# Performance work log

Hardware: AMD Instinct MI355X
Metric: run time of the kernel (lower is better)

## Reference

```python
import jax, jax.numpy as jnp
import numpy as np

H = 1024          # hidden_size
A = 8             # num_actions
T = 64            # timesteps
N = 256           # batch (num envs)


def _gru_cell(x, h, Wih, Whh, bih, bhh):
    # torch.nn.GRUCell math; gate order (r, z, n)
    gi = x @ Wih.T + bih           # [N, 3H]
    gh = h @ Whh.T + bhh           # [N, 3H]
    i_r, i_z, i_n = jnp.split(gi, 3, axis=1)
    h_r, h_z, h_n = jnp.split(gh, 3, axis=1)
    r = jax.nn.sigmoid(i_r + h_r)
    z = jax.nn.sigmoid(i_z + h_z)
    n = jnp.tanh(i_n + r * h_n)
    return (1.0 - z) * n + z * h


def setup_inputs() -> dict:
    key = jax.random.key(0)
    ks = jax.random.split(key, 12)
    s = 0.02
    return {
        "c": jax.random.normal(ks[0], (T * N, H), jnp.float32),
        "hxs": jax.random.normal(ks[1], (N, 3 * H), jnp.float32),
        "masks": jnp.ones((T * N, 1), jnp.float32),
        "prev_action_one_hot": jnp.zeros((T * N, A), jnp.float32).at[jnp.arange(T * N), jax.random.randint(ks[2], (T * N,), 0, A)].set(1.0),
        "h_gru_Wih": s * jax.random.normal(ks[3], (3 * H, H), jnp.float32),
        "h_gru_Whh": s * jax.random.normal(ks[4], (3 * H, H), jnp.float32),
        "h_gru_bih": jnp.zeros((3 * H,), jnp.float32),
        "h_gru_bhh": jnp.zeros((3 * H,), jnp.float32),
        "f_gru_Wih": s * jax.random.normal(ks[5], (3 * H, H), jnp.float32),
        "f_gru_Whh": s * jax.random.normal(ks[6], (3 * H, H), jnp.float32),
        "f_gru_bih": jnp.zeros((3 * H,), jnp.float32),
        "f_gru_bhh": jnp.zeros((3 * H,), jnp.float32),
        "p_W": s * jax.random.normal(ks[7], (2 * H, 2 * H + A), jnp.float32),
        "p_b": jnp.zeros((2 * H,), jnp.float32),
        "q_W": s * jax.random.normal(ks[8], (2 * H, 2 * H + A), jnp.float32),
        "q_b": jnp.zeros((2 * H,), jnp.float32),
    }


def reference(c, hxs, masks, prev_action_one_hot,
              h_gru_Wih, h_gru_Whh, h_gru_bih, h_gru_bhh,
              f_gru_Wih, f_gru_Whh, f_gru_bih, f_gru_bhh,
              p_W, p_b, q_W, q_b):
    c3 = c.reshape(T, N, H)
    m3 = masks.reshape(T, N, 1)
    a3 = prev_action_one_hot.reshape(T, N, A)
    f0 = hxs[:, :H]
    h0 = hxs[:, H:2 * H]
    q0 = hxs[:, 2 * H:]

    def step(carry, xs):
        f, h, q_mu = carry
        c_t, m_t, a_t = xs
        p_in = jnp.concatenate([h, q_mu, a_t], axis=1) * m_t
        p_dist = p_in @ p_W.T + p_b                     # [N, 2H]
        p_mu = p_dist[:, :H]
        q_in = jnp.concatenate([f, c_t, a_t], axis=1) * m_t
        q_dist = q_in @ q_W.T + q_b                     # [N, 2H]
        q_mu_new = q_dist[:, :H]
        f_new = _gru_cell(c_t, f * m_t, f_gru_Wih, f_gru_Whh, f_gru_bih, f_gru_bhh)
        h_new = _gru_cell(p_mu, h * m_t, h_gru_Wih, h_gru_Whh, h_gru_bih, h_gru_bhh)
        return (f_new, h_new, q_mu_new), (p_dist, q_dist)

    (f, h, q_mu), (p_all, q_all) = jax.lax.scan(step, (f0, h0, q0), (c3, m3, a3))
    acc_p = p_all.reshape(T * N, 2 * H)
    acc_q = q_all.reshape(T * N, 2 * H)
    hxs_out = jnp.concatenate([f, h, q_mu], axis=1)
    return acc_p, acc_q, hxs_out
```

## Files before the change

kernel.cpp:

```cpp
#include <hip/hip_runtime.h>
#include <math.h>

typedef __attribute__((ext_vector_type(8))) __bf16 bf16x8;
typedef __attribute__((ext_vector_type(4))) float f32x4;

constexpr int H = 1024, T = 64, NB = 256, TWOH = 2048, THREEH = 3072;
constexpr long long OFF_Q  = 33554432LL;
constexpr long long OFF_HX = 67108864LL;
constexpr int LA = 6;

constexpr int R_PWH = 0, R_PWQ = 2048, R_QWF = 4096, R_QWC = 6144,
              R_FWIH = 8192, R_FWHH = 11264, R_HWIH = 14336, R_HWHH = 17408;

#define LD4(p) (*reinterpret_cast<const float4*>(p))

__device__ __forceinline__ float sigf(float x) { return 1.0f / (1.0f + expf(-x)); }

__device__ __forceinline__ void gload16(const void* g, void* l) {
    __builtin_amdgcn_global_load_lds(
        (const __attribute__((address_space(1))) uint32_t*)g,
        (__attribute__((address_space(3))) uint32_t*)l, 16, 0, 0);
}

__device__ __forceinline__ void st_bf_swz(__bf16* base, int n, int k, float v) {
    base[(size_t)n * 1024 + (((k >> 3) ^ (n & 7)) << 3) + (k & 7)] = (__bf16)v;
}

#define FRAGOFF(rloc, gl) (((rloc) << 7) + ((((gl)) ^ ((rloc) & 7)) << 4))

template<int RT>
__device__ __forceinline__ void stage_tile(const char* g, char* l, int kb, int tid) {
    #pragma unroll
    for (int i = 0; i < RT / 32; ++i) {
        const int L = i * 4096 + tid * 16;
        gload16(g + (size_t)(L >> 7) * 2048 + (size_t)kb * 128 + (L & 127), l + L);
    }
}

__device__ __forceinline__ void mm128(
    int tid, char* sA, char* sB,
    const char* A0, const char* B0, int n0,
    const char* A1, const char* B1, int n1,
    f32x4 (&acc)[2][4])
{
    const int lane = tid & 63, w = tid >> 6;
    const int l15 = lane & 15, lg = lane >> 4;
    const int wr = w >> 1, wc = w & 1;
    const int nit = n0 + n1;
    int aoff[2][2], boff[4][2];
    #pragma unroll
    for (int fr = 0; fr < 2; ++fr)
        #pragma unroll
        for (int kk = 0; kk < 2; ++kk)
            aoff[fr][kk] = FRAGOFF(wr * 32 + fr * 16 + l15, kk * 4 + lg);
    #pragma unroll
    for (int fc = 0; fc < 4; ++fc)
        #pragma unroll
        for (int kk = 0; kk < 2; ++kk)
            boff[fc][kk] = FRAGOFF(wc * 64 + fc * 16 + l15, kk * 4 + lg);

    stage_tile<64>(A0, sA, 0, tid);
    stage_tile<128>(B0, sB, 0, tid);
    for (int kb = 0; kb < nit; ++kb) {
        const int kn = kb + 1;
        if (kn < nit) {
            const char* An = (kn < n0) ? A0 : A1;
            const char* Bn = (kn < n0) ? B0 : B1;
            const int kl = (kn < n0) ? kn : kn - n0;
            stage_tile<64>(An, sA + (kn & 1) * 8192, kl, tid);
            stage_tile<128>(Bn, sB + (kn & 1) * 16384, kl, tid);
            asm volatile("s_waitcnt vmcnt(6)" ::: "memory");
        } else {
            asm volatile("s_waitcnt vmcnt(0)" ::: "memory");
        }
        __builtin_amdgcn_s_barrier();
        __builtin_amdgcn_sched_barrier(0);
        char* Ab = sA + (kb & 1) * 8192;
        char* Bb = sB + (kb & 1) * 16384;
        bf16x8 af[2][2], bv[4][2];
        #pragma unroll
        for (int fr = 0; fr < 2; ++fr)
            #pragma unroll
            for (int kk = 0; kk < 2; ++kk)
                af[fr][kk] = *reinterpret_cast<const bf16x8*>(Ab + aoff[fr][kk]);
        #pragma unroll
        for (int fc = 0; fc < 4; ++fc)
            #pragma unroll
            for (int kk = 0; kk < 2; ++kk)
                bv[fc][kk] = *reinterpret_cast<const bf16x8*>(Bb + boff[fc][kk]);
        __builtin_amdgcn_s_setprio(1);
        #pragma unroll
        for (int kk = 0; kk < 2; ++kk)
            #pragma unroll
            for (int fr = 0; fr < 2; ++fr)
                #pragma unroll
                for (int fc = 0; fc < 4; ++fc)
                    acc[fr][fc] = __builtin_amdgcn_mfma_f32_16x16x32_bf16(
                        af[fr][kk], bv[fc][kk], acc[fr][fc], 0, 0, 0);
        __builtin_amdgcn_s_setprio(0);
        __builtin_amdgcn_s_barrier();
        __builtin_amdgcn_sched_barrier(0);
    }
}

__device__ __forceinline__ void mm32g1(
    int tid, char* sA, char* sB,
    const char* A, const char* Bg,
    f32x4 (&aR)[2], f32x4 (&aZ)[2], f32x4 (&aN)[2])
{
    const int lane = tid & 63, w = tid >> 6;
    const int l15 = lane & 15, lg = lane >> 4;
    const int wr = w >> 1, wc = w & 1;
    int aoff[2], boff[2][2];
    #pragma unroll
    for (int kk = 0; kk < 2; ++kk)
        aoff[kk] = FRAGOFF(wr * 16 + l15, kk * 4 + lg);
    #pragma unroll
    for (int fc = 0; fc < 2; ++fc)
        #pragma unroll
        for (int kk = 0; kk < 2; ++kk)
            boff[fc][kk] = FRAGOFF(wc * 32 + fc * 16 + l15, kk * 4 + lg);

    auto stg = [&](int buf, int kb) {
        stage_tile<32>(A, sA + buf * 4096, kb, tid);
        #pragma unroll
        for (int g = 0; g < 3; ++g)
            stage_tile<64>(Bg + (size_t)g * 2097152, sB + buf * 24576 + g * 8192, kb, tid);
    };
    stg(0, 0);
    for (int kb = 0; kb < 16; ++kb) {
        if (kb + 1 < 16) {
            stg((kb + 1) & 1, kb + 1);
            asm volatile("s_waitcnt vmcnt(7)" ::: "memory");
        } else {
            asm volatile("s_waitcnt vmcnt(0)" ::: "memory");
        }
        __builtin_amdgcn_s_barrier();
        __builtin_amdgcn_sched_barrier(0);
        char* Ab = sA + (kb & 1) * 4096;
        char* Bb = sB + (kb & 1) * 24576;
        bf16x8 af[2];
        #pragma unroll
        for (int kk = 0; kk < 2; ++kk)
            af[kk] = *reinterpret_cast<const bf16x8*>(Ab + aoff[kk]);
        bf16x8 bvr[2][2], bvz[2][2], bvn[2][2];
        #pragma unroll
        for (int fc = 0; fc < 2; ++fc)
            #pragma unroll
            for (int kk = 0; kk < 2; ++kk) {
                bvr[fc][kk] = *reinterpret_cast<const bf16x8*>(Bb + boff[fc][kk]);
                bvz[fc][kk] = *reinterpret_cast<const bf16x8*>(Bb + 8192 + boff[fc][kk]);
                bvn[fc][kk] = *reinterpret_cast<const bf16x8*>(Bb + 16384 + boff[fc][kk]);
            }
        __builtin_amdgcn_s_setprio(1);
        #pragma unroll
        for (int kk = 0; kk < 2; ++kk)
            #pragma unroll
            for (int fc = 0; fc < 2; ++fc) {
                aR[fc] = __builtin_amdgcn_mfma_f32_16x16x32_bf16(af[kk], bvr[fc][kk], aR[fc], 0, 0, 0);
                aZ[fc] = __builtin_amdgcn_mfma_f32_16x16x32_bf16(af[kk], bvz[fc][kk], aZ[fc], 0, 0, 0);
                aN[fc] = __builtin_amdgcn_mfma_f32_16x16x32_bf16(af[kk], bvn[fc][kk], aN[fc], 0, 0, 0);
            }
        __builtin_amdgcn_s_setprio(0);
        __builtin_amdgcn_s_barrier();
        __builtin_amdgcn_sched_barrier(0);
    }
}

__device__ __forceinline__ void do_xq(int slice, int i, int tid, char* sA, char* sB,
    const char* cbfB, const char* Wb, const float* act, const float* qW, float* out)
{
    const int lane = tid & 63, w = tid >> 6;
    const int l15 = lane & 15, lg = lane >> 4;
    const int wr = w >> 1, wc = w & 1;
    const int row0 = (i >> 4) * 64, col0 = (i & 15) * 128;
    const size_t grow0 = (size_t)slice * NB + row0;
    f32x4 acc[2][4] = {};
    mm128(tid, sA, sB, cbfB + grow0 * 2048, Wb + (size_t)(R_QWC + col0) * 2048, 16,
          nullptr, nullptr, 0, acc);
    #pragma unroll
    for (int fc = 0; fc < 4; ++fc) {
        const int gc = col0 + wc * 64 + fc * 16 + l15;
        const float* wp = qW + (size_t)gc * 2056 + 2048;
        float4 x0 = LD4(wp), x1 = LD4(wp + 4);
        #pragma unroll
        for (int fr = 0; fr < 2; ++fr)
            #pragma unroll
            for (int j = 0; j < 4; ++j) {
                const size_t n = grow0 + wr * 32 + fr * 16 + lg * 4 + j;
                const float* ar = act + n * 8;
                float4 a0 = LD4(ar), a1 = LD4(ar + 4);
                float dot = a0.x * x0.x + a0.y * x0.y + a0.z * x0.z + a0.w * x0.w
                          + a1.x * x1.x + a1.y * x1.y + a1.z * x1.z + a1.w * x1.w;
                out[OFF_Q + n * TWOH + gc] = acc[fr][fc][j] + dot;
            }
    }
}

__device__ __forceinline__ void do_gf(int slice, int i, int tid, char* sA, char* sB,
    const char* cbfB, const char* Wb, __bf16* Gfb)
{
    const int lane = tid & 63, w = tid >> 6;
    const int l15 = lane & 15, lg = lane >> 4;
    const int wr = w >> 1, wc = w & 1;
    const int row0 = (i / 24) * 64, col0 = (i % 24) * 128;
    f32x4 acc[2][4] = {};
    mm128(tid, sA, sB, cbfB + ((size_t)slice * NB + row0) * 2048,
          Wb + (size_t)(R_FWIH + col0) * 2048, 16, nullptr, nullptr, 0, acc);
    __bf16* gdst = Gfb + (size_t)(slice & 7) * NB * THREEH;
    #pragma unroll
    for (int fc = 0; fc < 4; ++fc) {
        const int gc = col0 + wc * 64 + fc * 16 + l15;
        #pragma unroll
        for (int fr = 0; fr < 2; ++fr)
            #pragma unroll
            for (int j = 0; j < 4; ++j) {
                const int n = row0 + wr * 32 + fr * 16 + lg * 4 + j;
                gdst[(size_t)n * THREEH + gc] = (__bf16)acc[fr][fc][j];
            }
    }
}

__global__ __launch_bounds__(256) void wcvt_k(
    const float* __restrict__ pW, const float* __restrict__ qW,
    const float* __restrict__ fWih, const float* __restrict__ fWhh,
    const float* __restrict__ hWih, const float* __restrict__ hWhh,
    __bf16* __restrict__ Wbf)
{
    const long i = (long)blockIdx.x * 256 + threadIdx.x;
    const int row = (int)(i >> 7);
    const int G   = (int)i & 127;
    const float* src; int stride; int koff = 0; int r;
    if (row < 2048)       { src = pW;   stride = 2056; koff = 0;    r = row; }
    else if (row < 4096)  { src = pW;   stride = 2056; koff = 1024; r = row - 2048; }
    else if (row < 6144)  { src = qW;   stride = 2056; koff = 0;    r = row - 4096; }
    else if (row < 8192)  { src = qW;   stride = 2056; koff = 1024; r = row - 6144; }
    else if (row < 11264) { src = fWih; stride = 1024; r = row - 8192; }
    else if (row < 14336) { src = fWhh; stride = 1024; r = row - 11264; }
    else if (row < 17408) { src = hWih; stride = 1024; r = row - 14336; }
    else                  { src = hWhh; stride = 1024; r = row - 17408; }
    const float* p = src + (long)r * stride + koff + G * 8;
    float4 a = LD4(p), b = LD4(p + 4);
    bf16x8 v;
    v[0] = (__bf16)a.x; v[1] = (__bf16)a.y; v[2] = (__bf16)a.z; v[3] = (__bf16)a.w;
    v[4] = (__bf16)b.x; v[5] = (__bf16)b.y; v[6] = (__bf16)b.z; v[7] = (__bf16)b.w;
    *reinterpret_cast<bf16x8*>(Wbf + (size_t)row * 1024 + ((G ^ (row & 7)) << 3)) = v;
}

__global__ __launch_bounds__(256) void ccvt_k(const float* __restrict__ c,
                                              __bf16* __restrict__ cbf) {
    const long i = (long)blockIdx.x * 256 + threadIdx.x;
    const int row = (int)(i >> 7);
    const int G   = (int)i & 127;
    const float* p = c + (size_t)row * 1024 + G * 8;
    float4 a = LD4(p), b = LD4(p + 4);
    bf16x8 v;
    v[0] = (__bf16)a.x; v[1] = (__bf16)a.y; v[2] = (__bf16)a.z; v[3] = (__bf16)a.w;
    v[4] = (__bf16)b.x; v[5] = (__bf16)b.y; v[6] = (__bf16)b.z; v[7] = (__bf16)b.w;
    *reinterpret_cast<bf16x8*>(cbf + (size_t)row * 1024 + ((G ^ (row & 7)) << 3)) = v;
}

__global__ __launch_bounds__(256) void init2_k(
    const float* __restrict__ hxs, const float* __restrict__ masks,
    float* __restrict__ fst0, float* __restrict__ hst0,
    __bf16* __restrict__ fbm0, __bf16* __restrict__ hbm0, __bf16* __restrict__ qmub0)
{
    const int idx = blockIdx.x * 256 + threadIdx.x;
    const int arr = idx >> 15;
    const int g   = idx & 32767;
    const int n   = g >> 7;
    const int G   = g & 127;
    const float m0 = masks[n];
    const float* p = hxs + (size_t)n * THREEH + arr * 1024 + G * 8;
    float4 a = LD4(p), b = LD4(p + 4);
    __bf16* dstB = arr == 0 ? fbm0 : (arr == 1 ? hbm0 : qmub0);
    bf16x8 v;
    v[0] = (__bf16)(a.x * m0); v[1] = (__bf16)(a.y * m0);
    v[2] = (__bf16)(a.z * m0); v[3] = (__bf16)(a.w * m0);
    v[4] = (__bf16)(b.x * m0); v[5] = (__bf16)(b.y * m0);
    v[6] = (__bf16)(b.z * m0); v[7] = (__bf16)(b.w * m0);
    *reinterpret_cast<bf16x8*>(dstB + (size_t)n * 1024 + ((G ^ (n & 7)) << 3)) = v;
    if (arr < 2) {
        float* dstF = arr == 0 ? fst0 : hst0;
        *reinterpret_cast<float4*>(dstF + (size_t)n * 1024 + G * 8) = a;
        *reinterpret_cast<float4*>(dstF + (size_t)n * 1024 + G * 8 + 4) = b;
    }
}

__global__ __launch_bounds__(256) void pre_k(
    const char* __restrict__ cbfB, const char* __restrict__ Wb,
    const float* __restrict__ act, const float* __restrict__ qW,
    __bf16* __restrict__ Gfb, float* __restrict__ out)
{
    __shared__ char smem[49152];
    const int s = blockIdx.x / 160;
    const int i = blockIdx.x % 160;
    if (i < 64) do_xq(s, i, threadIdx.x, smem, smem + 16384, cbfB, Wb, act, qW, out);
    else        do_gf(s, i - 64, threadIdx.x, smem, smem + 16384, cbfB, Wb, Gfb);
}

__global__ __launch_bounds__(256) void k1_k(
    int t, int hasFiller,
    const __bf16* __restrict__ hbm, const __bf16* __restrict__ qmub,
    __bf16* __restrict__ qmubN,
    const __bf16* __restrict__ fbm, const char* __restrict__ cbfB,
    const float* __restrict__ masks, const float* __restrict__ act,
    const float* __restrict__ pW, const float* __restrict__ pb,
    const float* __restrict__ qb, const float* __restrict__ qW,
    const char* __restrict__ Wb,
    __bf16* __restrict__ pmub, float* __restrict__ Shh, __bf16* __restrict__ Gfb,
    float* __restrict__ out)
{
    __shared__ char smem[49152];
    char* sA = smem;
    char* sB = smem + 16384;
    const int tid = threadIdx.x;
    const int lane = tid & 63, w = tid >> 6;
    const int l15 = lane & 15, lg = lane >> 4;
    const int wr = w >> 1, wc = w & 1;
    const float* mrow = masks + (size_t)t * NB;
    const float* mn   = masks + (size_t)(t + 1 < T ? t + 1 : t) * NB;
    int b = blockIdx.x;

    if (b < 64) {
        const int row0 = (b >> 4) * 64, col0 = (b & 15) * 128;
        f32x4 acc[2][4] = {};
        mm128(tid, sA, sB,
              (const char*)hbm + (size_t)row0 * 2048, Wb + (size_t)(R_PWH + col0) * 2048, 16,
              (const char*)qmub + (size_t)row0 * 2048, Wb + (size_t)(R_PWQ + col0) * 2048, 16,
              acc);
        float* ob = out + (size_t)t * NB * TWOH;
        #pragma unroll
        for (int fc = 0; fc < 4; ++fc) {
            const int gc = col0 + wc * 64 + fc * 16 + l15;
            const float* wp = pW + (size_t)gc * 2056 + 2048;
            float4 x0 = LD4(wp), x1 = LD4(wp + 4);
            const float bb = pb[gc];
            #pragma unroll
            for (int fr = 0; fr < 2; ++fr)
                #pragma unroll
                for (int j = 0; j < 4; ++j) {
                    const int n = row0 + wr * 32 + fr * 16 + lg * 4 + j;
                    const float* ar = act + ((size_t)t * NB + n) * 8;
                    float4 a0 = LD4(ar), a1 = LD4(ar + 4);
                    float dot = a0.x * x0.x + a0.y * x0.y + a0.z * x0.z + a0.w * x0.w
                              + a1.x * x1.x + a1.y * x1.y + a1.z * x1.z + a1.w * x1.w;
                    float v = acc[fr][fc][j] + mrow[n] * dot + bb;
                    ob[(size_t)n * TWOH + gc] = v;
                    if (gc < 1024) st_bf_swz(pmub, n, gc, v);
                }
        }
    } else if (b < 128) {
        b -= 64;
        const int row0 = (b >> 4) * 64, col0 = (b & 15) * 128;
        f32x4 acc[2][4] = {};
        mm128(tid, sA, sB,
              (const char*)fbm + (size_t)row0 * 2048, Wb + (size_t)(R_QWF + col0) * 2048, 16,
              nullptr, nullptr, 0, acc);
        float* ob = out + OFF_Q + (size_t)t * NB * TWOH;
        #pragma unroll
        for (int fc = 0; fc < 4; ++fc) {
            const int gc = col0 + wc * 64 + fc * 16 + l15;
            const float bb = qb[gc];
            #pragma unroll
            for (int fr = 0; fr < 2; ++fr)
                #pragma unroll
                for (int j = 0; j < 4; ++j) {
                    const int n = row0 + wr * 32 + fr * 16 + lg * 4 + j;
                    const float xq = ob[(size_t)n * TWOH + gc];
                    float v = acc[fr][fc][j] + mrow[n] * xq + bb;
                    ob[(size_t)n * TWOH + gc] = v;
                    if (gc < 1024) st_bf_swz(qmubN, n, gc, v * mn[n]);
                }
        }
    } else if (b < 224) {
        const int i = b - 128;
        const int row0 = (i / 24) * 64, col0 = (i % 24) * 128;
        f32x4 acc[2][4] = {};
        mm128(tid, sA, sB,
              (const char*)hbm + (size_t)row0 * 2048, Wb + (size_t)(R_HWHH + col0) * 2048, 16,
              nullptr, nullptr, 0, acc);
        #pragma unroll
        for (int fc = 0; fc < 4; ++fc) {
            const int gc = col0 + wc * 64 + fc * 16 + l15;
            #pragma unroll
            for (int fr = 0; fr < 2; ++fr)
                #pragma unroll
                for (int j = 0; j < 4; ++j) {
                    const int n = row0 + wr * 32 + fr * 16 + lg * 4 + j;
                    Shh[(size_t)n * THREEH + gc] = acc[fr][fc][j];
                }
        }
    } else if (b < 288) {
        if (hasFiller) do_xq(t + LA, b - 224, tid, sA, sB, cbfB, Wb, act, qW, out);
    } else {
        if (hasFiller) do_gf(t + LA, b - 288, tid, sA, sB, cbfB, Wb, Gfb);
    }
}

__global__ __launch_bounds__(256) void k2_k(
    int t,
    const __bf16* __restrict__ pmub, const __bf16* __restrict__ hbm,
    const __bf16* __restrict__ fbm,
    const float* __restrict__ Shh, const __bf16* __restrict__ Gfb,
    const float* __restrict__ hstF, float* __restrict__ hstN, __bf16* __restrict__ hbmN,
    const float* __restrict__ fstF, float* __restrict__ fstN, __bf16* __restrict__ fbmN,
    const char* __restrict__ Wb,
    const float* __restrict__ hbih, const float* __restrict__ hbhh,
    const float* __restrict__ fbih, const float* __restrict__ fbhh,
    const float* __restrict__ masks)
{
    __shared__ char smem[57344];
    char* sA = smem;
    char* sB = smem + 8192;
    const int tid = threadIdx.x;
    const int lane = tid & 63, w = tid >> 6;
    const int l15 = lane & 15, lg = lane >> 4;
    const int wr = w >> 1, wc = w & 1;
    const float* mrow = masks + (size_t)t * NB;
    const float* mn   = masks + (size_t)(t + 1 < T ? t + 1 : t) * NB;
    const int b = blockIdx.x;
    const int i = b & 127;
    const int row0 = (i >> 4) * 32, col0 = (i & 15) * 64;

    f32x4 aR[2] = {}, aZ[2] = {}, aN[2] = {};
    if (b < 128) {
        mm32g1(tid, sA, sB,
               (const char*)pmub + (size_t)row0 * 2048,
               Wb + (size_t)(R_HWIH + col0) * 2048, aR, aZ, aN);
        #pragma unroll
        for (int fc = 0; fc < 2; ++fc) {
            const int col = col0 + wc * 32 + fc * 16 + l15;
            const float bri = hbih[col],        brh = hbhh[col];
            const float bzi = hbih[col + 1024], bzh = hbhh[col + 1024];
            const float bni = hbih[col + 2048], bnh = hbhh[col + 2048];
            #pragma unroll
            for (int j = 0; j < 4; ++j) {
                const int n = row0 + wr * 16 + lg * 4 + j;
                const float ghr = Shh[(size_t)n * THREEH + col];
                const float ghz = Shh[(size_t)n * THREEH + col + 1024];
                const float ghn = Shh[(size_t)n * THREEH + col + 2048];
                const float rg = sigf(aR[fc][j] + bri + ghr + brh);
                const float zg = sigf(aZ[fc][j] + bzi + ghz + bzh);
                const float ng = tanhf(aN[fc][j] + bni + rg * (ghn + bnh));
                const float hm = hstF[(size_t)n * 1024 + col] * mrow[n];
                const float o = (1.f - zg) * ng + zg * hm;
                hstN[(size_t)n * 1024 + col] = o;
                st_bf_swz(hbmN, n, col, o * mn[n]);
            }
        }
    } else {
        mm32g1(tid, sA, sB,
               (const char*)fbm + (size_t)row0 * 2048,
               Wb + (size_t)(R_FWHH + col0) * 2048, aR, aZ, aN);
        const __bf16* gsl = Gfb + (size_t)(t & 7) * NB * THREEH;
        #pragma unroll
        for (int fc = 0; fc < 2; ++fc) {
            const int col = col0 + wc * 32 + fc * 16 + l15;
            const float br  = fbih[col] + fbhh[col];
            const float bz  = fbih[col + 1024] + fbhh[col + 1024];
            const float bni = fbih[col + 2048], bnh = fbhh[col + 2048];
            #pragma unroll
            for (int j = 0; j < 4; ++j) {
                const int n = row0 + wr * 16 + lg * 4 + j;
                const float gfr = (float)gsl[(size_t)n * THREEH + col];
                const float gfz = (float)gsl[(size_t)n * THREEH + col + 1024];
                const float gfn = (float)gsl[(size_t)n * THREEH + col + 2048];
                const float rg = sigf(gfr + aR[fc][j] + br);
                const float zg = sigf(gfz + aZ[fc][j] + bz);
                const float ng = tanhf(gfn + bni + rg * (aN[fc][j] + bnh));
                const float fm = fstF[(size_t)n * 1024 + col] * mrow[n];
                const float o = (1.f - zg) * ng + zg * fm;
                fstN[(size_t)n * 1024 + col] = o;
                st_bf_swz(fbmN, n, col, o * mn[n]);
            }
        }
    }
}

__global__ __launch_bounds__(256) void write_hxs_k(const float* __restrict__ fS,
                                                   const float* __restrict__ hS,
                                                   float* out) {
    const int i = blockIdx.x * 256 + threadIdx.x;
    const int n = i / THREEH;
    const int j = i - n * THREEH;
    float v;
    if (j < H)          v = fS[(size_t)n * H + j];
    else if (j < TWOH)  v = hS[(size_t)n * H + (j - H)];
    else                v = out[OFF_Q + ((size_t)(T - 1) * NB + n) * TWOH + (j - TWOH)];
    out[OFF_HX + i] = v;
}

extern "C" void kernel_launch(void* const* d_in, const int* in_sizes, int n_in,
                              void* d_out, int out_size, void* d_ws, size_t ws_size,
                              hipStream_t stream) {
    (void)in_sizes; (void)n_in; (void)out_size; (void)ws_size;

    const float* c     = (const float*)d_in[0];
    const float* hxs   = (const float*)d_in[1];
    const float* masks = (const float*)d_in[2];
    const float* act   = (const float*)d_in[3];
    const float* hWih  = (const float*)d_in[4];
    const float* hWhh  = (const float*)d_in[5];
    const float* hbih  = (const float*)d_in[6];
    const float* hbhh  = (const float*)d_in[7];
    const float* fWih  = (const float*)d_in[8];
    const float* fWhh  = (const float*)d_in[9];
    const float* fbih  = (const float*)d_in[10];
    const float* fbhh  = (const float*)d_in[11];
    const float* pW    = (const float*)d_in[12];
    const float* pb    = (const float*)d_in[13];
    const float* qW    = (const float*)d_in[14];
    const float* qb    = (const float*)d_in[15];

    float* out = (float*)d_out;
    char*  wsb = (char*)d_ws;

    __bf16* Wbf  = (__bf16*)(wsb);
    __bf16* cbf  = (__bf16*)(wsb + 41943040LL);
    float*  fst[2] = { (float*)(wsb + 75497472LL), (float*)(wsb + 76546048LL) };
    float*  hst[2] = { (float*)(wsb + 77594624LL), (float*)(wsb + 78643200LL) };
    __bf16* fbm[2] = { (__bf16*)(wsb + 79691776LL), (__bf16*)(wsb + 80216064LL) };
    __bf16* hbm[2] = { (__bf16*)(wsb + 80740352LL), (__bf16*)(wsb + 81264640LL) };
    __bf16* qmb[2] = { (__bf16*)(wsb + 81788928LL), (__bf16*)(wsb + 82313216LL) };
    __bf16* pmub   = (__bf16*)(wsb + 82837504LL);
    float*  Shh    = (float*)(wsb + 83361792LL);
    __bf16* Gfb    = (__bf16*)(wsb + 86507520LL);
    const char* Wb = (const char*)Wbf;
    const char* cbfB = (const char*)cbf;

    wcvt_k <<<dim3(10240), dim3(256), 0, stream>>>(pW, qW, fWih, fWhh, hWih, hWhh, Wbf);
    ccvt_k <<<dim3(8192),  dim3(256), 0, stream>>>(c, cbf);
    init2_k<<<dim3(384),   dim3(256), 0, stream>>>(hxs, masks, fst[0], hst[0],
                                                   fbm[0], hbm[0], qmb[0]);
    pre_k  <<<dim3(LA * 160), dim3(256), 0, stream>>>(cbfB, Wb, act, qW, Gfb, out);

    for (int t = 0; t < T; ++t) {
        const int cur = t & 1, nxt = cur ^ 1;
        const int hasF = (t + LA < T) ? 1 : 0;
        k1_k<<<dim3(hasF ? 384 : 224), dim3(256), 0, stream>>>(
            t, hasF, hbm[cur], qmb[cur], qmb[nxt], fbm[cur], cbfB,
            masks, act, pW, pb, qb, qW, Wb, pmub, Shh, Gfb, out);
        k2_k<<<dim3(256), dim3(256), 0, stream>>>(
            t, pmub, hbm[cur], fbm[cur], Shh, Gfb,
            hst[cur], hst[nxt], hbm[nxt],
            fst[cur], fst[nxt], fbm[nxt],
            Wb, hbih, hbhh, fbih, fbhh, masks);
    }

    write_hxs_k<<<dim3(3072), dim3(256), 0, stream>>>(fst[0], hst[0], out);
}
```

Before: 2.271 ms.

## Fold p_W into h-GRU input weights and merge per-step kernels into one

Precomputes the products of the h-GRU input weights with the p_W blocks (for h, q_mu, the action columns and the bias) so the h-GRU input gates come straight from h and q_mu with K=3072. This removes the dependency on p_mu within a timestep, so the two per-step launches (k1, k2) collapse into a single step kernel. The Shh and pmub round trips through global memory also go away. The cost is extra precompute kernels, a larger per-step GEMM for the h-GRU blocks, and an additional bf16 rounding of the composed weights that may shift numerics.

```diff
diff --git a/kernel.cpp b/kernel.cpp
--- a/kernel.cpp
+++ b/kernel.cpp
@@ -103,18 +103,24 @@
     }
 }
 
-__device__ __forceinline__ void mm32g1(
+__device__ __forceinline__ void mm64g(
     int tid, char* sA, char* sB,
-    const char* A, const char* Bg,
-    f32x4 (&aR)[2], f32x4 (&aZ)[2], f32x4 (&aN)[2])
+    const char* A0, const char* B0,
+    const char* A1, const char* B1,
+    const char* A2, const char* B2,
+    int nseg, int nhMask,
+    f32x4 (&aR)[2][2], f32x4 (&aZ)[2][2], f32x4 (&aNi)[2][2], f32x4 (&aNh)[2][2])
 {
     const int lane = tid & 63, w = tid >> 6;
     const int l15 = lane & 15, lg = lane >> 4;
     const int wr = w >> 1, wc = w & 1;
-    int aoff[2], boff[2][2];
-    #pragma unroll
-    for (int kk = 0; kk < 2; ++kk)
-        aoff[kk] = FRAGOFF(wr * 16 + l15, kk * 4 + lg);
+    const int nit = nseg * 16;
+    int aoff[2][2], boff[2][2];
+    #pragma unroll
+    for (int fr = 0; fr < 2; ++fr)
+        #pragma unroll
+        for (int kk = 0; kk < 2; ++kk)
+            aoff[fr][kk] = FRAGOFF(wr * 32 + fr * 16 + l15, kk * 4 + lg);
     #pragma unroll
     for (int fc = 0; fc < 2; ++fc)
         #pragma unroll
@@ -122,27 +128,32 @@
             boff[fc][kk] = FRAGOFF(wc * 32 + fc * 16 + l15, kk * 4 + lg);
 
     auto stg = [&](int buf, int kb) {
-        stage_tile<32>(A, sA + buf * 4096, kb, tid);
+        const int seg = kb >> 4, kl = kb & 15;
+        const char* Ag = (seg == 0) ? A0 : ((seg == 1) ? A1 : A2);
+        const char* Bg = (seg == 0) ? B0 : ((seg == 1) ? B1 : B2);
+        stage_tile<64>(Ag, sA + buf * 8192, kl, tid);
         #pragma unroll
         for (int g = 0; g < 3; ++g)
-            stage_tile<64>(Bg + (size_t)g * 2097152, sB + buf * 24576 + g * 8192, kb, tid);
+            stage_tile<64>(Bg + (size_t)g * 2097152, sB + buf * 24576 + g * 8192, kl, tid);
     };
     stg(0, 0);
-    for (int kb = 0; kb < 16; ++kb) {
-        if (kb + 1 < 16) {
+    for (int kb = 0; kb < nit; ++kb) {
+        if (kb + 1 < nit) {
             stg((kb + 1) & 1, kb + 1);
-            asm volatile("s_waitcnt vmcnt(7)" ::: "memory");
+            asm volatile("s_waitcnt vmcnt(8)" ::: "memory");
         } else {
             asm volatile("s_waitcnt vmcnt(0)" ::: "memory");
         }
         __builtin_amdgcn_s_barrier();
         __builtin_amdgcn_sched_barrier(0);
-        char* Ab = sA + (kb & 1) * 4096;
+        char* Ab = sA + (kb & 1) * 8192;
         char* Bb = sB + (kb & 1) * 24576;
-        bf16x8 af[2];
-        #pragma unroll
-        for (int kk = 0; kk < 2; ++kk)
-            af[kk] = *reinterpret_cast<const bf16x8*>(Ab + aoff[kk]);
+        bf16x8 af[2][2];
+        #pragma unroll
+        for (int fr = 0; fr < 2; ++fr)
+            #pragma unroll
+            for (int kk = 0; kk < 2; ++kk)
+                af[fr][kk] = *reinterpret_cast<const bf16x8*>(Ab + aoff[fr][kk]);
         bf16x8 bvr[2][2], bvz[2][2], bvn[2][2];
         #pragma unroll
         for (int fc = 0; fc < 2; ++fc)
@@ -152,15 +163,38 @@
                 bvz[fc][kk] = *reinterpret_cast<const bf16x8*>(Bb + 8192 + boff[fc][kk]);
                 bvn[fc][kk] = *reinterpret_cast<const bf16x8*>(Bb + 16384 + boff[fc][kk]);
             }
+        const bool toNh = (nhMask >> (kb >> 4)) & 1;
         __builtin_amdgcn_s_setprio(1);
         #pragma unroll
         for (int kk = 0; kk < 2; ++kk)
             #pragma unroll
-            for (int fc = 0; fc < 2; ++fc) {
-                aR[fc] = __builtin_amdgcn_mfma_f32_16x16x32_bf16(af[kk], bvr[fc][kk], aR[fc], 0, 0, 0);
-                aZ[fc] = __builtin_amdgcn_mfma_f32_16x16x32_bf16(af[kk], bvz[fc][kk], aZ[fc], 0, 0, 0);
-                aN[fc] = __builtin_amdgcn_mfma_f32_16x16x32_bf16(af[kk], bvn[fc][kk], aN[fc], 0, 0, 0);
-            }
+            for (int fr = 0; fr < 2; ++fr)
+                #pragma unroll
+                for (int fc = 0; fc < 2; ++fc) {
+                    aR[fr][fc] = __builtin_amdgcn_mfma_f32_16x16x32_bf16(
+                        af[fr][kk], bvr[fc][kk], aR[fr][fc], 0, 0, 0);
+                    aZ[fr][fc] = __builtin_amdgcn_mfma_f32_16x16x32_bf16(
+                        af[fr][kk], bvz[fc][kk], aZ[fr][fc], 0, 0, 0);
+                }
+        if (toNh) {
+            #pragma unroll
+            for (int kk = 0; kk < 2; ++kk)
+                #pragma unroll
+                for (int fr = 0; fr < 2; ++fr)
+                    #pragma unroll
+                    for (int fc = 0; fc < 2; ++fc)
+                        aNh[fr][fc] = __builtin_amdgcn_mfma_f32_16x16x32_bf16(
+                            af[fr][kk], bvn[fc][kk], aNh[fr][fc], 0, 0, 0);
+        } else {
+            #pragma unroll
+            for (int kk = 0; kk < 2; ++kk)
+                #pragma unroll
+                for (int fr = 0; fr < 2; ++fr)
+                    #pragma unroll
+                    for (int fc = 0; fc < 2; ++fc)
+                        aNi[fr][fc] = __builtin_amdgcn_mfma_f32_16x16x32_bf16(
+                            af[fr][kk], bvn[fc][kk], aNi[fr][fc], 0, 0, 0);
+        }
         __builtin_amdgcn_s_setprio(0);
         __builtin_amdgcn_s_barrier();
         __builtin_amdgcn_sched_barrier(0);
@@ -258,6 +292,91 @@
     v[0] = (__bf16)a.x; v[1] = (__bf16)a.y; v[2] = (__bf16)a.z; v[3] = (__bf16)a.w;
     v[4] = (__bf16)b.x; v[5] = (__bf16)b.y; v[6] = (__bf16)b.z; v[7] = (__bf16)b.w;
     *reinterpret_cast<bf16x8*>(cbf + (size_t)row * 1024 + ((G ^ (row & 7)) << 3)) = v;
+}
+
+__global__ __launch_bounds__(256) void pwt_k(const float* __restrict__ pW,
+                                             __bf16* __restrict__ pWT) {
+    __shared__ float lds[64][65];
+    const int t = threadIdx.x;
+    const int i0 = blockIdx.y * 64, j0 = blockIdx.x * 64;
+    const int ir = t >> 4, jc = (t & 15) * 4;
+    #pragma unroll
+    for (int rr = 0; rr < 4; ++rr) {
+        const int il = rr * 16 + ir;
+        float4 v = LD4(pW + (size_t)(i0 + il) * 2056 + j0 + jc);
+        lds[jc + 0][il] = v.x; lds[jc + 1][il] = v.y;
+        lds[jc + 2][il] = v.z; lds[jc + 3][il] = v.w;
+    }
+    __syncthreads();
+    #pragma unroll
+    for (int ww = 0; ww < 2; ++ww) {
+        const int jl = ww * 32 + (t >> 3);
+        const int g8 = t & 7;
+        bf16x8 v;
+        #pragma unroll
+        for (int u = 0; u < 8; ++u) v[u] = (__bf16)lds[jl][g8 * 8 + u];
+        const int j = j0 + jl;
+        const int G = (i0 >> 3) + g8;
+        *reinterpret_cast<bf16x8*>(pWT + (size_t)j * 1024 + ((G ^ (j & 7)) << 3)) = v;
+    }
+}
+
+__global__ __launch_bounds__(256) void comp_k(const char* __restrict__ Wb,
+                                              const char* __restrict__ pWTb,
+                                              __bf16* __restrict__ Ch,
+                                              __bf16* __restrict__ Cq) {
+    __shared__ char smem[49152];
+    const int tid = threadIdx.x;
+    const int lane = tid & 63, w = tid >> 6;
+    const int l15 = lane & 15, lg = lane >> 4;
+    const int wr = w >> 1, wc = w & 1;
+    const int row0 = (blockIdx.x >> 4) * 64;
+    const int col0 = (blockIdx.x & 15) * 128;
+    f32x4 acc[2][4] = {};
+    mm128(tid, smem, smem + 16384,
+          Wb + (size_t)(R_HWIH + row0) * 2048, pWTb + (size_t)col0 * 2048, 16,
+          nullptr, nullptr, 0, acc);
+    #pragma unroll
+    for (int fc = 0; fc < 4; ++fc) {
+        const int j = col0 + wc * 64 + fc * 16 + l15;
+        #pragma unroll
+        for (int fr = 0; fr < 2; ++fr)
+            #pragma unroll
+            for (int jj = 0; jj < 4; ++jj) {
+                const int g = row0 + wr * 32 + fr * 16 + lg * 4 + jj;
+                const float v = acc[fr][fc][jj];
+                if (j < 1024) st_bf_swz(Ch, g, j, v);
+                else          st_bf_swz(Cq, g, j - 1024, v);
+            }
+    }
+}
+
+__global__ __launch_bounds__(256) void ca_k(const float* __restrict__ hWih,
+                                            const float* __restrict__ pW,
+                                            const float* __restrict__ pb,
+                                            float* __restrict__ Ca,
+                                            float* __restrict__ cbv) {
+    const int g = blockIdx.x * 4 + (threadIdx.x >> 6);
+    const int l = threadIdx.x & 63;
+    float s[9] = {};
+    for (int it = 0; it < 16; ++it) {
+        const int i = l + it * 64;
+        const float hw = hWih[(size_t)g * 1024 + i];
+        const float* pr = pW + (size_t)i * 2056 + 2048;
+        float4 x0 = LD4(pr), x1 = LD4(pr + 4);
+        s[0] += hw * x0.x; s[1] += hw * x0.y; s[2] += hw * x0.z; s[3] += hw * x0.w;
+        s[4] += hw * x1.x; s[5] += hw * x1.y; s[6] += hw * x1.z; s[7] += hw * x1.w;
+        s[8] += hw * pb[i];
+    }
+    #pragma unroll
+    for (int off = 32; off >= 1; off >>= 1)
+        #pragma unroll
+        for (int u = 0; u < 9; ++u) s[u] += __shfl_down(s[u], off);
+    if (l == 0) {
+        #pragma unroll
+        for (int u = 0; u < 8; ++u) Ca[(size_t)g * 8 + u] = s[u];
+        cbv[g] = s[8];
+    }
 }
 
 __global__ __launch_bounds__(256) void init2_k(
@@ -299,7 +418,7 @@
     else        do_gf(s, i - 64, threadIdx.x, smem, smem + 16384, cbfB, Wb, Gfb);
 }
 
-__global__ __launch_bounds__(256) void k1_k(
+__global__ __launch_bounds__(256) void step_k(
     int t, int hasFiller,
     const __bf16* __restrict__ hbm, const __bf16* __restrict__ qmub,
     __bf16* __restrict__ qmubN,
@@ -307,11 +426,16 @@
     const float* __restrict__ masks, const float* __restrict__ act,
     const float* __restrict__ pW, const float* __restrict__ pb,
     const float* __restrict__ qb, const float* __restrict__ qW,
-    const char* __restrict__ Wb,
-    __bf16* __restrict__ pmub, float* __restrict__ Shh, __bf16* __restrict__ Gfb,
-    float* __restrict__ out)
-{
-    __shared__ char smem[49152];
+    const char* __restrict__ Wb, const char* __restrict__ ChB,
+    const char* __restrict__ CqB,
+    const float* __restrict__ Ca, const float* __restrict__ cbv,
+    const float* __restrict__ hstF, float* __restrict__ hstN, __bf16* __restrict__ hbmN,
+    const float* __restrict__ fstF, float* __restrict__ fstN, __bf16* __restrict__ fbmN,
+    const float* __restrict__ hbih, const float* __restrict__ hbhh,
+    const float* __restrict__ fbih, const float* __restrict__ fbhh,
+    __bf16* __restrict__ Gfb, float* __restrict__ out)
+{
+    __shared__ char smem[65536];
     char* sA = smem;
     char* sB = smem + 16384;
     const int tid = threadIdx.x;
@@ -345,9 +469,7 @@
                     float4 a0 = LD4(ar), a1 = LD4(ar + 4);
                     float dot = a0.x * x0.x + a0.y * x0.y + a0.z * x0.z + a0.w * x0.w
                               + a1.x * x1.x + a1.y * x1.y + a1.z * x1.z + a1.w * x1.w;
-                    float v = acc[fr][fc][j] + mrow[n] * dot + bb;
-                    ob[(size_t)n * TWOH + gc] = v;
-                    if (gc < 1024) st_bf_swz(pmub, n, gc, v);
+                    ob[(size_t)n * TWOH + gc] = acc[fr][fc][j] + mrow[n] * dot + bb;
                 }
         }
     } else if (b < 128) {
@@ -373,86 +495,60 @@
                     if (gc < 1024) st_bf_swz(qmubN, n, gc, v * mn[n]);
                 }
         }
-    } else if (b < 224) {
+    } else if (b < 192) {
         const int i = b - 128;
-        const int row0 = (i / 24) * 64, col0 = (i % 24) * 128;
-        f32x4 acc[2][4] = {};
-        mm128(tid, sA, sB,
-              (const char*)hbm + (size_t)row0 * 2048, Wb + (size_t)(R_HWHH + col0) * 2048, 16,
-              nullptr, nullptr, 0, acc);
-        #pragma unroll
-        for (int fc = 0; fc < 4; ++fc) {
-            const int gc = col0 + wc * 64 + fc * 16 + l15;
+        const int row0 = (i >> 4) * 64, col0 = (i & 15) * 64;
+        f32x4 aR[2][2] = {}, aZ[2][2] = {}, aNi[2][2] = {}, aNh[2][2] = {};
+        mm64g(tid, sA, sB,
+              (const char*)hbm + (size_t)row0 * 2048, ChB + (size_t)col0 * 2048,
+              (const char*)hbm + (size_t)row0 * 2048, Wb + (size_t)(R_HWHH + col0) * 2048,
+              (const char*)qmub + (size_t)row0 * 2048, CqB + (size_t)col0 * 2048,
+              3, 0b010, aR, aZ, aNi, aNh);
+        #pragma unroll
+        for (int fc = 0; fc < 2; ++fc) {
+            const int col = col0 + wc * 32 + fc * 16 + l15;
+            const float cbr = cbv[col]        + hbih[col]        + hbhh[col];
+            const float cbz = cbv[col + 1024] + hbih[col + 1024] + hbhh[col + 1024];
+            const float cbn = cbv[col + 2048] + hbih[col + 2048];
+            const float bnh = hbhh[col + 2048];
+            const float* car = Ca + (size_t)col * 8;
+            const float* caz = Ca + (size_t)(col + 1024) * 8;
+            const float* can = Ca + (size_t)(col + 2048) * 8;
+            float4 r0 = LD4(car), r1 = LD4(car + 4);
+            float4 z0 = LD4(caz), z1 = LD4(caz + 4);
+            float4 n0 = LD4(can), n1 = LD4(can + 4);
             #pragma unroll
             for (int fr = 0; fr < 2; ++fr)
                 #pragma unroll
                 for (int j = 0; j < 4; ++j) {
                     const int n = row0 + wr * 32 + fr * 16 + lg * 4 + j;
-                    Shh[(size_t)n * THREEH + gc] = acc[fr][fc][j];
+                    const float m = mrow[n];
+                    const float* ar = act + ((size_t)t * NB + n) * 8;
+                    float4 a0 = LD4(ar), a1 = LD4(ar + 4);
+                    const float dr = a0.x*r0.x + a0.y*r0.y + a0.z*r0.z + a0.w*r0.w
+                                   + a1.x*r1.x + a1.y*r1.y + a1.z*r1.z + a1.w*r1.w;
+                    const float dz = a0.x*z0.x + a0.y*z0.y + a0.z*z0.z + a0.w*z0.w
+                                   + a1.x*z1.x + a1.y*z1.y + a1.z*z1.z + a1.w*z1.w;
+                    const float dn = a0.x*n0.x + a0.y*n0.y + a0.z*n0.z + a0.w*n0.w
+                                   + a1.x*n1.x + a1.y*n1.y + a1.z*n1.z + a1.w*n1.w;
+                    const float rg = sigf(aR[fr][fc][j] + m * dr + cbr);
+                    const float zg = sigf(aZ[fr][fc][j] + m * dz + cbz);
+                    const float ng = tanhf(aNi[fr][fc][j] + m * dn + cbn
+                                           + rg * (aNh[fr][fc][j] + bnh));
+                    const float hm = hstF[(size_t)n * 1024 + col] * m;
+                    const float o = (1.f - zg) * ng + zg * hm;
+                    hstN[(size_t)n * 1024 + col] = o;
+                    st_bf_swz(hbmN, n, col, o * mn[n]);
                 }
         }
-    } else if (b < 288) {
-        if (hasFiller) do_xq(t + LA, b - 224, tid, sA, sB, cbfB, Wb, act, qW, out);
-    } else {
-        if (hasFiller) do_gf(t + LA, b - 288, tid, sA, sB, cbfB, Wb, Gfb);
-    }
-}
-
-__global__ __launch_bounds__(256) void k2_k(
-    int t,
-    const __bf16* __restrict__ pmub, const __bf16* __restrict__ hbm,
-    const __bf16* __restrict__ fbm,
-    const float* __restrict__ Shh, const __bf16* __restrict__ Gfb,
-    const float* __restrict__ hstF, float* __restrict__ hstN, __bf16* __restrict__ hbmN,
-    const float* __restrict__ fstF, float* __restrict__ fstN, __bf16* __restrict__ fbmN,
-    const char* __restrict__ Wb,
-    const float* __restrict__ hbih, const float* __restrict__ hbhh,
-    const float* __restrict__ fbih, const float* __restrict__ fbhh,
-    const float* __restrict__ masks)
-{
-    __shared__ char smem[57344];
-    char* sA = smem;
-    char* sB = smem + 8192;
-    const int tid = threadIdx.x;
-    const int lane = tid & 63, w = tid >> 6;
-    const int l15 = lane & 15, lg = lane >> 4;
-    const int wr = w >> 1, wc = w & 1;
-    const float* mrow = masks + (size_t)t * NB;
-    const float* mn   = masks + (size_t)(t + 1 < T ? t + 1 : t) * NB;
-    const int b = blockIdx.x;
-    const int i = b & 127;
-    const int row0 = (i >> 4) * 32, col0 = (i & 15) * 64;
-
-    f32x4 aR[2] = {}, aZ[2] = {}, aN[2] = {};
-    if (b < 128) {
-        mm32g1(tid, sA, sB,
-               (const char*)pmub + (size_t)row0 * 2048,
-               Wb + (size_t)(R_HWIH + col0) * 2048, aR, aZ, aN);
-        #pragma unroll
-        for (int fc = 0; fc < 2; ++fc) {
-            const int col = col0 + wc * 32 + fc * 16 + l15;
-            const float bri = hbih[col],        brh = hbhh[col];
-            const float bzi = hbih[col + 1024], bzh = hbhh[col + 1024];
-            const float bni = hbih[col + 2048], bnh = hbhh[col + 2048];
-            #pragma unroll
-            for (int j = 0; j < 4; ++j) {
-                const int n = row0 + wr * 16 + lg * 4 + j;
-                const float ghr = Shh[(size_t)n * THREEH + col];
-                const float ghz = Shh[(size_t)n * THREEH + col + 1024];
-                const float ghn = Shh[(size_t)n * THREEH + col + 2048];
-                const float rg = sigf(aR[fc][j] + bri + ghr + brh);
-                const float zg = sigf(aZ[fc][j] + bzi + ghz + bzh);
-                const float ng = tanhf(aN[fc][j] + bni + rg * (ghn + bnh));
-                const float hm = hstF[(size_t)n * 1024 + col] * mrow[n];
-                const float o = (1.f - zg) * ng + zg * hm;
-                hstN[(size_t)n * 1024 + col] = o;
-                st_bf_swz(hbmN, n, col, o * mn[n]);
-            }
-        }
-    } else {
-        mm32g1(tid, sA, sB,
-               (const char*)fbm + (size_t)row0 * 2048,
-               Wb + (size_t)(R_FWHH + col0) * 2048, aR, aZ, aN);
+    } else if (b < 256) {
+        const int i = b - 192;
+        const int row0 = (i >> 4) * 64, col0 = (i & 15) * 64;
+        f32x4 aR[2][2] = {}, aZ[2][2] = {}, aNi[2][2] = {}, aNh[2][2] = {};
+        mm64g(tid, sA, sB,
+              (const char*)fbm + (size_t)row0 * 2048, Wb + (size_t)(R_FWHH + col0) * 2048,
+              nullptr, nullptr, nullptr, nullptr,
+              1, 0b001, aR, aZ, aNi, aNh);
         const __bf16* gsl = Gfb + (size_t)(t & 7) * NB * THREEH;
         #pragma unroll
         for (int fc = 0; fc < 2; ++fc) {
@@ -461,20 +557,26 @@
             const float bz  = fbih[col + 1024] + fbhh[col + 1024];
             const float bni = fbih[col + 2048], bnh = fbhh[col + 2048];
             #pragma unroll
-            for (int j = 0; j < 4; ++j) {
-                const int n = row0 + wr * 16 + lg * 4 + j;
-                const float gfr = (float)gsl[(size_t)n * THREEH + col];
-                const float gfz = (float)gsl[(size_t)n * THREEH + col + 1024];
-                const float gfn = (float)gsl[(size_t)n * THREEH + col + 2048];
-                const float rg = sigf(gfr + aR[fc][j] + br);
-                const float zg = sigf(gfz + aZ[fc][j] + bz);
-                const float ng = tanhf(gfn + bni + rg * (aN[fc][j] + bnh));
-                const float fm = fstF[(size_t)n * 1024 + col] * mrow[n];
-                const float o = (1.f - zg) * ng + zg * fm;
-                fstN[(size_t)n * 1024 + col] = o;
-                st_bf_swz(fbmN, n, col, o * mn[n]);
-            }
+            for (int fr = 0; fr < 2; ++fr)
+                #pragma unroll
+                for (int j = 0; j < 4; ++j) {
+                    const int n = row0 + wr * 32 + fr * 16 + lg * 4 + j;
+                    const float gfr = (float)gsl[(size_t)n * THREEH + col];
+                    const float gfz = (float)gsl[(size_t)n * THREEH + col + 1024];
+                    const float gfn = (float)gsl[(size_t)n * THREEH + col + 2048];
+                    const float rg = sigf(gfr + aR[fr][fc][j] + br);
+                    const float zg = sigf(gfz + aZ[fr][fc][j] + bz);
+                    const float ng = tanhf(gfn + bni + rg * (aNh[fr][fc][j] + bnh));
+                    const float fm = fstF[(size_t)n * 1024 + col] * mrow[n];
+                    const float o = (1.f - zg) * ng + zg * fm;
+                    fstN[(size_t)n * 1024 + col] = o;
+                    st_bf_swz(fbmN, n, col, o * mn[n]);
+                }
         }
+    } else if (b < 320) {
+        if (hasFiller) do_xq(t + LA, b - 256, tid, sA, sB, cbfB, Wb, act, qW, out);
+    } else {
+        if (hasFiller) do_gf(t + LA, b - 320, tid, sA, sB, cbfB, Wb, Gfb);
     }
 }
 
@@ -523,29 +625,34 @@
     __bf16* fbm[2] = { (__bf16*)(wsb + 79691776LL), (__bf16*)(wsb + 80216064LL) };
     __bf16* hbm[2] = { (__bf16*)(wsb + 80740352LL), (__bf16*)(wsb + 81264640LL) };
     __bf16* qmb[2] = { (__bf16*)(wsb + 81788928LL), (__bf16*)(wsb + 82313216LL) };
-    __bf16* pmub   = (__bf16*)(wsb + 82837504LL);
-    float*  Shh    = (float*)(wsb + 83361792LL);
-    __bf16* Gfb    = (__bf16*)(wsb + 86507520LL);
-    const char* Wb = (const char*)Wbf;
+    __bf16* pWT    = (__bf16*)(wsb + 82837504LL);
+    __bf16* Chbuf  = (__bf16*)(wsb + 87031808LL);
+    __bf16* Cqbuf  = (__bf16*)(wsb + 93323264LL);
+    float*  Ca     = (float*)(wsb + 99614720LL);
+    float*  cbv    = (float*)(wsb + 99713024LL);
+    __bf16* Gfb    = (__bf16*)(wsb + 99725312LL);
+    const char* Wb   = (const char*)Wbf;
     const char* cbfB = (const char*)cbf;
 
     wcvt_k <<<dim3(10240), dim3(256), 0, stream>>>(pW, qW, fWih, fWhh, hWih, hWhh, Wbf);
     ccvt_k <<<dim3(8192),  dim3(256), 0, stream>>>(c, cbf);
+    pwt_k  <<<dim3(32, 16), dim3(256), 0, stream>>>(pW, pWT);
     init2_k<<<dim3(384),   dim3(256), 0, stream>>>(hxs, masks, fst[0], hst[0],
                                                    fbm[0], hbm[0], qmb[0]);
+    comp_k <<<dim3(768), dim3(256), 0, stream>>>(Wb, (const char*)pWT, Chbuf, Cqbuf);
+    ca_k   <<<dim3(768), dim3(256), 0, stream>>>(hWih, pW, pb, Ca, cbv);
     pre_k  <<<dim3(LA * 160), dim3(256), 0, stream>>>(cbfB, Wb, act, qW, Gfb, out);
 
     for (int t = 0; t < T; ++t) {
         const int cur = t & 1, nxt = cur ^ 1;
         const int hasF = (t + LA < T) ? 1 : 0;
-        k1_k<<<dim3(hasF ? 384 : 224), dim3(256), 0, stream>>>(
+        step_k<<<dim3(hasF ? 416 : 256), dim3(256), 0, stream>>>(
             t, hasF, hbm[cur], qmb[cur], qmb[nxt], fbm[cur], cbfB,
-            masks, act, pW, pb, qb, qW, Wb, pmub, Shh, Gfb, out);
-        k2_k<<<dim3(256), dim3(256), 0, stream>>>(
-            t, pmub, hbm[cur], fbm[cur], Shh, Gfb,
+            masks, act, pW, pb, qb, qW,
+            Wb, (const char*)Chbuf, (const char*)Cqbuf, Ca, cbv,
             hst[cur], hst[nxt], hbm[nxt],
             fst[cur], fst[nxt], fbm[nxt],
-            Wb, hbih, hbhh, fbih, fbhh, masks);
+            hbih, hbhh, fbih, fbhh, Gfb, out);
     }
 
     write_hxs_k<<<dim3(3072), dim3(256), 0, stream>>>(fst[0], hst[0], out);
```

After: 6.238 ms. +174.7%, slower.
